# Optimization experiments

Measured on AMD Instinct MI355X. Metric: run time of the kernel, lower is better.

The kernel has to match this reference:

```python
import jax, jax.numpy as jnp
import numpy as np

N_HEADS = 16
D_K = 64
D_V = 64
HIDDEN = 1024
B, S = 2, 2048
LN_EPS = 1e-5


def setup_inputs() -> dict:
    key = jax.random.key(0)
    ks = jax.random.split(key, 6)
    inputs = jax.random.normal(ks[0], (B, S, HIDDEN), dtype=jnp.float32)
    attn_mask = jax.random.randint(ks[1], (B, S, S), 0, 2, dtype=jnp.int32)
    scale = 1.0 / np.sqrt(HIDDEN)
    W_Q = jax.random.normal(ks[2], (HIDDEN, HIDDEN), dtype=jnp.float32) * scale
    W_K = jax.random.normal(ks[3], (HIDDEN, HIDDEN), dtype=jnp.float32) * scale
    W_V = jax.random.normal(ks[4], (HIDDEN, HIDDEN), dtype=jnp.float32) * scale
    W_O = jax.random.normal(ks[5], (HIDDEN, HIDDEN), dtype=jnp.float32) * scale
    return {"inputs": inputs, "attn_mask": attn_mask,
            "W_Q": W_Q, "W_K": W_K, "W_V": W_V, "W_O": W_O}


def reference(inputs, attn_mask, W_Q, W_K, W_V, W_O):
    b, s, _ = inputs.shape
    # nn.Linear(bias=False): x @ W.T ; reshape to [B, H, S, d]
    Q = (inputs @ W_Q.T).reshape(b, s, N_HEADS, D_K).transpose(0, 2, 1, 3)
    K = (inputs @ W_K.T).reshape(b, s, N_HEADS, D_K).transpose(0, 2, 1, 3)
    V = (inputs @ W_V.T).reshape(b, s, N_HEADS, D_V).transpose(0, 2, 1, 3)
    scores = jnp.einsum('bhqd,bhkd->bhqk', Q, K) / np.sqrt(D_K)
    mask = (attn_mask == 0)[:, None, :, :]  # broadcast over heads
    scores = jnp.where(mask, jnp.float32(-1e9), scores)
    attn = jax.nn.softmax(scores, axis=-1)
    context = jnp.einsum('bhqk,bhkd->bhqd', attn, V)
    context = context.transpose(0, 2, 1, 3).reshape(b, s, N_HEADS * D_V)
    output = context @ W_O.T
    x = output + inputs  # residual
    # LayerNorm with default weight=1, bias=0, eps=1e-5
    mu = jnp.mean(x, axis=-1, keepdims=True)
    var = jnp.mean(jnp.square(x - mu), axis=-1, keepdims=True)
    out = (x - mu) * jax.lax.rsqrt(var + LN_EPS)
    return out, attn
```

## Files before the change

kernel.cpp:

```cpp
#include <hip/hip_runtime.h>

typedef unsigned short u16;
typedef unsigned long long u64;
typedef __bf16 bf16x8 __attribute__((ext_vector_type(8)));
typedef float f32x4 __attribute__((ext_vector_type(4)));

static __device__ __forceinline__ u16 f32_to_bf16(float f) {
    unsigned u = __builtin_bit_cast(unsigned, f);
    u += 0x7fffu + ((u >> 16) & 1u);
    return (u16)(u >> 16);
}
static __device__ __forceinline__ float bf16_to_f32(u16 v) {
    return __builtin_bit_cast(float, ((unsigned)v) << 16);
}

__global__ __launch_bounds__(256) void cast_f32_bf16(const float* __restrict__ in,
                                                     u16* __restrict__ out, int n)
{
    int i = (blockIdx.x * 256 + threadIdx.x) * 4;
    if (i >= n) return;
    float4 v = *reinterpret_cast<const float4*>(in + i);
    ushort4 o;
    o.x = f32_to_bf16(v.x); o.y = f32_to_bf16(v.y);
    o.z = f32_to_bf16(v.z); o.w = f32_to_bf16(v.w);
    *reinterpret_cast<ushort4*>(out + i) = o;
}

__global__ __launch_bounds__(256) void cast_w4(
    const float* __restrict__ w0, const float* __restrict__ w1,
    const float* __restrict__ w2, const float* __restrict__ w3,
    u16* __restrict__ o0, u16* __restrict__ o1,
    u16* __restrict__ o2, u16* __restrict__ o3)
{
    const float* src; u16* dst;
    switch (blockIdx.y) {
        case 0: src = w0; dst = o0; break;
        case 1: src = w1; dst = o1; break;
        case 2: src = w2; dst = o2; break;
        default: src = w3; dst = o3; break;
    }
    int i = (blockIdx.x * 256 + threadIdx.x) * 4;
    float4 v = *reinterpret_cast<const float4*>(src + i);
    ushort4 o;
    o.x = f32_to_bf16(v.x); o.y = f32_to_bf16(v.y);
    o.z = f32_to_bf16(v.z); o.w = f32_to_bf16(v.w);
    *reinterpret_cast<ushort4*>(dst + i) = o;
}

__global__ __launch_bounds__(256) void pack_mask(const int* __restrict__ mask,
                                                 u64* __restrict__ out)
{
    int t = blockIdx.x * 256 + threadIdx.x;
    const int4* p = reinterpret_cast<const int4*>(mask + (size_t)t * 64);
    u64 bits = 0;
#pragma unroll
    for (int j = 0; j < 16; ++j) {
        int4 v = p[j];
        bits |= ((u64)(v.x != 0)) << (j * 4 + 0);
        bits |= ((u64)(v.y != 0)) << (j * 4 + 1);
        bits |= ((u64)(v.z != 0)) << (j * 4 + 2);
        bits |= ((u64)(v.w != 0)) << (j * 4 + 3);
    }
    out[t] = bits;
}

__global__ __launch_bounds__(256) void gemm128_qkv(
    const u16* __restrict__ A,
    const u16* __restrict__ BQ, const u16* __restrict__ BK, const u16* __restrict__ BV,
    u16* __restrict__ CQ, u16* __restrict__ CK, u16* __restrict__ CV)
{
    constexpr int N = 1024, K = 1024;
    const u16* B; u16* C;
    switch (blockIdx.z) {
        case 0:  B = BQ; C = CQ; break;
        case 1:  B = BK; C = CK; break;
        default: B = BV; C = CV; break;
    }
    __shared__ __align__(16) u16 As[128][72];
    __shared__ __align__(16) u16 Bs[128][72];
    const int tid  = threadIdx.x;
    const int wave = tid >> 6, lane = tid & 63;
    const int quad = lane >> 4, l16 = lane & 15;
    const int wr = wave >> 1, wc = wave & 1;
    const int m0 = blockIdx.y * 128, n0 = blockIdx.x * 128;

    f32x4 acc[4][4] = {};
    const int r0 = tid >> 3;
    const int c0 = (tid & 7) * 8;
    const u16* Ap = A + (size_t)(m0 + r0) * K + c0;
    const u16* Bp = B + (size_t)(n0 + r0) * K + c0;

    for (int k0 = 0; k0 < K; k0 += 64) {
        __syncthreads();
#pragma unroll
        for (int i = 0; i < 4; ++i) {
            *reinterpret_cast<int4*>(&As[r0 + 32 * i][c0]) =
                *reinterpret_cast<const int4*>(Ap + (size_t)(32 * i) * K + k0);
            *reinterpret_cast<int4*>(&Bs[r0 + 32 * i][c0]) =
                *reinterpret_cast<const int4*>(Bp + (size_t)(32 * i) * K + k0);
        }
        __syncthreads();
#pragma unroll
        for (int ks = 0; ks < 2; ++ks) {
            bf16x8 a[4], bb[4];
#pragma unroll
            for (int mi = 0; mi < 4; ++mi)
                a[mi] = *reinterpret_cast<const bf16x8*>(&As[wr * 64 + mi * 16 + l16][ks * 32 + quad * 8]);
#pragma unroll
            for (int ni = 0; ni < 4; ++ni)
                bb[ni] = *reinterpret_cast<const bf16x8*>(&Bs[wc * 64 + ni * 16 + l16][ks * 32 + quad * 8]);
#pragma unroll
            for (int mi = 0; mi < 4; ++mi)
#pragma unroll
                for (int ni = 0; ni < 4; ++ni)
                    acc[mi][ni] = __builtin_amdgcn_mfma_f32_16x16x32_bf16(a[mi], bb[ni], acc[mi][ni], 0, 0, 0);
        }
    }
#pragma unroll
    for (int mi = 0; mi < 4; ++mi)
#pragma unroll
        for (int ni = 0; ni < 4; ++ni)
#pragma unroll
            for (int r = 0; r < 4; ++r) {
                int row = m0 + wr * 64 + mi * 16 + quad * 4 + r;
                int col = n0 + wc * 64 + ni * 16 + l16;
                C[(size_t)row * N + col] = f32_to_bf16(acc[mi][ni][r]);
            }
}

__global__ __launch_bounds__(256) void gemm128_res(
    const u16* __restrict__ A, const u16* __restrict__ B,
    const float* __restrict__ X, float* __restrict__ C)
{
    constexpr int N = 1024, K = 1024;
    __shared__ __align__(16) u16 As[128][72];
    __shared__ __align__(16) u16 Bs[128][72];
    const int tid  = threadIdx.x;
    const int wave = tid >> 6, lane = tid & 63;
    const int quad = lane >> 4, l16 = lane & 15;
    const int wr = wave >> 1, wc = wave & 1;
    const int m0 = blockIdx.y * 128, n0 = blockIdx.x * 128;

    f32x4 acc[4][4] = {};
    const int r0 = tid >> 3;
    const int c0 = (tid & 7) * 8;
    const u16* Ap = A + (size_t)(m0 + r0) * K + c0;
    const u16* Bp = B + (size_t)(n0 + r0) * K + c0;

    for (int k0 = 0; k0 < K; k0 += 64) {
        __syncthreads();
#pragma unroll
        for (int i = 0; i < 4; ++i) {
            *reinterpret_cast<int4*>(&As[r0 + 32 * i][c0]) =
                *reinterpret_cast<const int4*>(Ap + (size_t)(32 * i) * K + k0);
            *reinterpret_cast<int4*>(&Bs[r0 + 32 * i][c0]) =
                *reinterpret_cast<const int4*>(Bp + (size_t)(32 * i) * K + k0);
        }
        __syncthreads();
#pragma unroll
        for (int ks = 0; ks < 2; ++ks) {
            bf16x8 a[4], bb[4];
#pragma unroll
            for (int mi = 0; mi < 4; ++mi)
                a[mi] = *reinterpret_cast<const bf16x8*>(&As[wr * 64 + mi * 16 + l16][ks * 32 + quad * 8]);
#pragma unroll
            for (int ni = 0; ni < 4; ++ni)
                bb[ni] = *reinterpret_cast<const bf16x8*>(&Bs[wc * 64 + ni * 16 + l16][ks * 32 + quad * 8]);
#pragma unroll
            for (int mi = 0; mi < 4; ++mi)
#pragma unroll
                for (int ni = 0; ni < 4; ++ni)
                    acc[mi][ni] = __builtin_amdgcn_mfma_f32_16x16x32_bf16(a[mi], bb[ni], acc[mi][ni], 0, 0, 0);
        }
    }
#pragma unroll
    for (int mi = 0; mi < 4; ++mi)
#pragma unroll
        for (int ni = 0; ni < 4; ++ni)
#pragma unroll
            for (int r = 0; r < 4; ++r) {
                int row = m0 + wr * 64 + mi * 16 + quad * 4 + r;
                int col = n0 + wc * 64 + ni * 16 + l16;
                C[(size_t)row * N + col] = acc[mi][ni][r] + X[(size_t)row * N + col];
            }
}

__global__ __launch_bounds__(256) void transpose_v(const u16* __restrict__ Vw,
                                                   u16* __restrict__ VT)
{
    constexpr int S = 2048, HID = 1024, NH = 16;
    __shared__ __align__(16) u16 Ts[64][72];
    const int tid = threadIdx.x;
    const int lr = tid >> 2, lc = (tid & 3) * 16;
    const int st = blockIdx.x, h = blockIdx.y, b = blockIdx.z;
    {
        const u16* p = Vw + ((size_t)(b * S + st * 64 + lr)) * HID + h * 64 + lc;
        *reinterpret_cast<int4*>(&Ts[lr][lc])     = *reinterpret_cast<const int4*>(p);
        *reinterpret_cast<int4*>(&Ts[lr][lc + 8]) = *reinterpret_cast<const int4*>(p + 8);
    }
    __syncthreads();
    u16* q = VT + ((size_t)((b * NH + h) * 64 + lr)) * S + st * 64 + lc;
    union { int4 v; u16 s[8]; } o0, o1;
#pragma unroll
    for (int j = 0; j < 8; ++j) o0.s[j] = Ts[lc + j][lr];
#pragma unroll
    for (int j = 0; j < 8; ++j) o1.s[j] = Ts[lc + 8 + j][lr];
    *reinterpret_cast<int4*>(q)     = o0.v;
    *reinterpret_cast<int4*>(q + 8) = o1.v;
}

__global__ __launch_bounds__(256) void attn_kernel(
    const u16* __restrict__ Q, const u16* __restrict__ K,
    const u16* __restrict__ VT, const u64* __restrict__ Mb,
    float* __restrict__ attn_out, u16* __restrict__ ctx_out)
{
    constexpr int S = 2048, HID = 1024, NH = 16;
    __shared__ __align__(16) u16 Qs[64][72];
    __shared__ __align__(16) u16 Ks[64][72];
    __shared__ __align__(16) u16 Vs[64][72];
    __shared__ __align__(16) u16 Ps[64][72];

    const int tid  = threadIdx.x;
    const int wave = tid >> 6, lane = tid & 63;
    const int quad = lane >> 4, l16 = lane & 15;
    const int qt = blockIdx.x, h = blockIdx.y, b = blockIdx.z;
    const size_t qkv_base = (size_t)b * S * HID + h * 64;
    const size_t vt_base  = ((size_t)(b * NH + h)) * 64 * S;

    const int lr = tid >> 2;
    const int lc = (tid & 3) * 16;
    {
        const u16* p = Q + qkv_base + (size_t)(qt * 64 + lr) * HID + lc;
        *reinterpret_cast<int4*>(&Qs[lr][lc])     = *reinterpret_cast<const int4*>(p);
        *reinterpret_cast<int4*>(&Qs[lr][lc + 8]) = *reinterpret_cast<const int4*>(p + 8);
    }

    float m_i[4], l_i[4];
#pragma unroll
    for (int r = 0; r < 4; ++r) { m_i[r] = -1e30f; l_i[r] = 0.f; }

    const int q_row0 = qt * 64 + wave * 16 + quad * 4;
    const size_t mrow = (size_t)b * S + q_row0;

    for (int kt = 0; kt < S / 64; ++kt) {
        u64 mw[4];
#pragma unroll
        for (int r = 0; r < 4; ++r) mw[r] = Mb[(mrow + r) * 32 + kt];
        __syncthreads();
        {
            const u16* p = K + qkv_base + (size_t)(kt * 64 + lr) * HID + lc;
            *reinterpret_cast<int4*>(&Ks[lr][lc])     = *reinterpret_cast<const int4*>(p);
            *reinterpret_cast<int4*>(&Ks[lr][lc + 8]) = *reinterpret_cast<const int4*>(p + 8);
        }
        __syncthreads();
        f32x4 sc[4] = {};
#pragma unroll
        for (int ks = 0; ks < 2; ++ks) {
            bf16x8 a = *reinterpret_cast<const bf16x8*>(&Qs[wave * 16 + l16][ks * 32 + quad * 8]);
#pragma unroll
            for (int cb = 0; cb < 4; ++cb) {
                bf16x8 bb = *reinterpret_cast<const bf16x8*>(&Ks[cb * 16 + l16][ks * 32 + quad * 8]);
                sc[cb] = __builtin_amdgcn_mfma_f32_16x16x32_bf16(a, bb, sc[cb], 0, 0, 0);
            }
        }
        float s_val[4][4];
#pragma unroll
        for (int cb = 0; cb < 4; ++cb) {
            int bi = cb * 16 + l16;
#pragma unroll
            for (int r = 0; r < 4; ++r)
                s_val[cb][r] = ((mw[r] >> bi) & 1ull) ? sc[cb][r] * 0.125f : -1e9f;
        }
#pragma unroll
        for (int r = 0; r < 4; ++r) {
            float mx = fmaxf(fmaxf(s_val[0][r], s_val[1][r]), fmaxf(s_val[2][r], s_val[3][r]));
            mx = fmaxf(mx, __shfl_xor(mx, 1));
            mx = fmaxf(mx, __shfl_xor(mx, 2));
            mx = fmaxf(mx, __shfl_xor(mx, 4));
            mx = fmaxf(mx, __shfl_xor(mx, 8));
            float m_new = fmaxf(m_i[r], mx);
            float sum = 0.f;
#pragma unroll
            for (int cb = 0; cb < 4; ++cb) sum += __expf(s_val[cb][r] - m_new);
            sum += __shfl_xor(sum, 1);
            sum += __shfl_xor(sum, 2);
            sum += __shfl_xor(sum, 4);
            sum += __shfl_xor(sum, 8);
            l_i[r] = l_i[r] * __expf(m_i[r] - m_new) + sum;
            m_i[r] = m_new;
        }
    }
    float rl[4];
#pragma unroll
    for (int r = 0; r < 4; ++r) rl[r] = 1.0f / l_i[r];

    f32x4 ctx[4] = {};
    for (int kt = 0; kt < S / 64; ++kt) {
        u64 mw[4];
#pragma unroll
        for (int r = 0; r < 4; ++r) mw[r] = Mb[(mrow + r) * 32 + kt];
        __syncthreads();
        {
            const u16* p = K + qkv_base + (size_t)(kt * 64 + lr) * HID + lc;
            *reinterpret_cast<int4*>(&Ks[lr][lc])     = *reinterpret_cast<const int4*>(p);
            *reinterpret_cast<int4*>(&Ks[lr][lc + 8]) = *reinterpret_cast<const int4*>(p + 8);
            const u16* pv = VT + vt_base + (size_t)lr * S + kt * 64 + lc;
            *reinterpret_cast<int4*>(&Vs[lr][lc])     = *reinterpret_cast<const int4*>(pv);
            *reinterpret_cast<int4*>(&Vs[lr][lc + 8]) = *reinterpret_cast<const int4*>(pv + 8);
        }
        __syncthreads();
        f32x4 sc[4] = {};
#pragma unroll
        for (int ks = 0; ks < 2; ++ks) {
            bf16x8 a = *reinterpret_cast<const bf16x8*>(&Qs[wave * 16 + l16][ks * 32 + quad * 8]);
#pragma unroll
            for (int cb = 0; cb < 4; ++cb) {
                bf16x8 bb = *reinterpret_cast<const bf16x8*>(&Ks[cb * 16 + l16][ks * 32 + quad * 8]);
                sc[cb] = __builtin_amdgcn_mfma_f32_16x16x32_bf16(a, bb, sc[cb], 0, 0, 0);
            }
        }
#pragma unroll
        for (int cb = 0; cb < 4; ++cb) {
            int bi = cb * 16 + l16;
#pragma unroll
            for (int r = 0; r < 4; ++r) {
                float s = ((mw[r] >> bi) & 1ull) ? sc[cb][r] * 0.125f : -1e9f;
                float pval = __expf(s - m_i[r]) * rl[r];
                Ps[wave * 16 + quad * 4 + r][cb * 16 + l16] = f32_to_bf16(pval);
            }
        }
        __syncthreads();
        {
            size_t arow = (((size_t)(b * NH + h) * S) + qt * 64 + lr) * S + kt * 64 + lc;
#pragma unroll
            for (int g = 0; g < 4; ++g) {
                float4 o;
                o.x = bf16_to_f32(Ps[lr][lc + g * 4 + 0]);
                o.y = bf16_to_f32(Ps[lr][lc + g * 4 + 1]);
                o.z = bf16_to_f32(Ps[lr][lc + g * 4 + 2]);
                o.w = bf16_to_f32(Ps[lr][lc + g * 4 + 3]);
                *reinterpret_cast<float4*>(&attn_out[arow + g * 4]) = o;
            }
        }
#pragma unroll
        for (int ks = 0; ks < 2; ++ks) {
            bf16x8 a = *reinterpret_cast<const bf16x8*>(&Ps[wave * 16 + l16][ks * 32 + quad * 8]);
#pragma unroll
            for (int cb = 0; cb < 4; ++cb) {
                bf16x8 bb = *reinterpret_cast<const bf16x8*>(&Vs[cb * 16 + l16][ks * 32 + quad * 8]);
                ctx[cb] = __builtin_amdgcn_mfma_f32_16x16x32_bf16(a, bb, ctx[cb], 0, 0, 0);
            }
        }
    }
#pragma unroll
    for (int cb = 0; cb < 4; ++cb)
#pragma unroll
        for (int r = 0; r < 4; ++r) {
            int q = q_row0 + r;
            int d = cb * 16 + l16;
            ctx_out[qkv_base + (size_t)q * HID + d] = f32_to_bf16(ctx[cb][r]);
        }
}

__global__ __launch_bounds__(256) void ln_kernel(const float* __restrict__ X,
                                                 float* __restrict__ out)
{
    __shared__ float red[8];
    const int row = blockIdx.x;
    const int tid = threadIdx.x;
    const int wave = tid >> 6, lane = tid & 63;
    const float* xr = X + (size_t)row * 1024;
    float v[4];
    float s = 0.f;
#pragma unroll
    for (int i = 0; i < 4; ++i) { v[i] = xr[tid + 256 * i]; s += v[i]; }
#pragma unroll
    for (int off = 1; off < 64; off <<= 1) s += __shfl_xor(s, off);
    if (lane == 0) red[wave] = s;
    __syncthreads();
    float mean = (red[0] + red[1] + red[2] + red[3]) * (1.0f / 1024.0f);
    float s2 = 0.f;
#pragma unroll
    for (int i = 0; i < 4; ++i) { float d = v[i] - mean; s2 += d * d; }
#pragma unroll
    for (int off = 1; off < 64; off <<= 1) s2 += __shfl_xor(s2, off);
    if (lane == 0) red[4 + wave] = s2;
    __syncthreads();
    float var = (red[4] + red[5] + red[6] + red[7]) * (1.0f / 1024.0f);
    float rstd = rsqrtf(var + 1e-5f);
#pragma unroll
    for (int i = 0; i < 4; ++i)
        out[(size_t)row * 1024 + tid + 256 * i] = (v[i] - mean) * rstd;
}

extern "C" void kernel_launch(void* const* d_in, const int* in_sizes, int n_in,
                              void* d_out, int out_size, void* d_ws, size_t ws_size,
                              hipStream_t stream)
{
    constexpr int B = 2, S = 2048, HID = 1024, NH = 16;
    constexpr int M = B * S;

    const float* X  = (const float*)d_in[0];
    const int* mask = (const int*)d_in[1];
    const float* WQ = (const float*)d_in[2];
    const float* WK = (const float*)d_in[3];
    const float* WV = (const float*)d_in[4];
    const float* WO = (const float*)d_in[5];

    float* out  = (float*)d_out;
    float* attn = out + (size_t)M * HID;

    u64*   Mb  = (u64*)d_ws;
    u16*   Xb  = (u16*)(Mb + (size_t)B * S * 32);
    u16*   WQb = Xb  + (size_t)M * HID;
    u16*   WKb = WQb + (size_t)HID * HID;
    u16*   WVb = WKb + (size_t)HID * HID;
    u16*   WOb = WVb + (size_t)HID * HID;
    u16*   Qw  = WOb + (size_t)HID * HID;
    u16*   Kw  = Qw  + (size_t)M * HID;
    u16*   Vw  = Kw  + (size_t)M * HID;
    u16*   Cw  = Vw  + (size_t)M * HID;
    u16*   VT  = Xb;
    float* XO  = (float*)Qw;

    dim3 blk(256);
    cast_f32_bf16<<<dim3((M * HID) / 1024), blk, 0, stream>>>(X, Xb, M * HID);
    cast_w4<<<dim3((HID * HID) / 1024, 4), blk, 0, stream>>>(WQ, WK, WV, WO,
                                                             WQb, WKb, WVb, WOb);
    pack_mask<<<dim3((B * S * 32) / 256), blk, 0, stream>>>(mask, Mb);

    gemm128_qkv<<<dim3(HID / 128, M / 128, 3), blk, 0, stream>>>(Xb, WQb, WKb, WVb,
                                                                 Qw, Kw, Vw);
    transpose_v<<<dim3(S / 64, NH, B), blk, 0, stream>>>(Vw, VT);

    attn_kernel<<<dim3(S / 64, NH, B), blk, 0, stream>>>(Qw, Kw, VT, Mb, attn, Cw);

    gemm128_res<<<dim3(HID / 128, M / 128), blk, 0, stream>>>(Cw, WOb, X, XO);
    ln_kernel<<<dim3(M), blk, 0, stream>>>(XO, out);
}
```

Before: 889.3 us.

## Prefetch next K/V tiles into registers and swizzle block order across XCDs

The attention kernel now issues the global loads for the next K (and V) tile into registers before computing on the current tile, so memory latency overlaps with the MFMA and softmax work. It also remaps the flat block index so that consecutive hardware block IDs, which are spread round-robin across the chip's chiplets, correspond to nearby (batch, head, q-tile) work. The aim is better L2 locality for the K/V data shared by q-tiles of the same head. The cost is extra live registers for the prefetched tiles, which could lower occupancy.

```diff
diff --git a/kernel.cpp b/kernel.cpp
--- a/kernel.cpp
+++ b/kernel.cpp
@@ -223,7 +223,11 @@
     const int tid  = threadIdx.x;
     const int wave = tid >> 6, lane = tid & 63;
     const int quad = lane >> 4, l16 = lane & 15;
-    const int qt = blockIdx.x, h = blockIdx.y, b = blockIdx.z;
+
+    const int flat = (blockIdx.z * NH + blockIdx.y) * (S / 64) + blockIdx.x;
+    const int s_id = (flat & 7) * 128 + (flat >> 3);
+    const int qt = s_id & 31, h = (s_id >> 5) & 15, b = s_id >> 9;
+
     const size_t qkv_base = (size_t)b * S * HID + h * 64;
     const size_t vt_base  = ((size_t)(b * NH + h)) * 64 * S;
 
@@ -242,16 +246,24 @@
     const int q_row0 = qt * 64 + wave * 16 + quad * 4;
     const size_t mrow = (size_t)b * S + q_row0;
 
+    const u16* Kp = K + qkv_base + (size_t)lr * HID + lc;
+    const u16* Vp = VT + vt_base + (size_t)lr * S + lc;
+
+    int4 kc0 = *reinterpret_cast<const int4*>(Kp);
+    int4 kc1 = *reinterpret_cast<const int4*>(Kp + 8);
     for (int kt = 0; kt < S / 64; ++kt) {
         u64 mw[4];
 #pragma unroll
         for (int r = 0; r < 4; ++r) mw[r] = Mb[(mrow + r) * 32 + kt];
         __syncthreads();
-        {
-            const u16* p = K + qkv_base + (size_t)(kt * 64 + lr) * HID + lc;
-            *reinterpret_cast<int4*>(&Ks[lr][lc])     = *reinterpret_cast<const int4*>(p);
-            *reinterpret_cast<int4*>(&Ks[lr][lc + 8]) = *reinterpret_cast<const int4*>(p + 8);
-        }
+        *reinterpret_cast<int4*>(&Ks[lr][lc])     = kc0;
+        *reinterpret_cast<int4*>(&Ks[lr][lc + 8]) = kc1;
+        int4 kn0, kn1;
+        if (kt < S / 64 - 1) {
+            const u16* p = Kp + (size_t)(kt + 1) * 64 * HID;
+            kn0 = *reinterpret_cast<const int4*>(p);
+            kn1 = *reinterpret_cast<const int4*>(p + 8);
+        } else { kn0 = kc0; kn1 = kc1; }
         __syncthreads();
         f32x4 sc[4] = {};
 #pragma unroll
@@ -289,25 +301,35 @@
             l_i[r] = l_i[r] * __expf(m_i[r] - m_new) + sum;
             m_i[r] = m_new;
         }
+        kc0 = kn0; kc1 = kn1;
     }
     float rl[4];
 #pragma unroll
     for (int r = 0; r < 4; ++r) rl[r] = 1.0f / l_i[r];
 
     f32x4 ctx[4] = {};
+    kc0 = *reinterpret_cast<const int4*>(Kp);
+    kc1 = *reinterpret_cast<const int4*>(Kp + 8);
+    int4 vc0 = *reinterpret_cast<const int4*>(Vp);
+    int4 vc1 = *reinterpret_cast<const int4*>(Vp + 8);
     for (int kt = 0; kt < S / 64; ++kt) {
         u64 mw[4];
 #pragma unroll
         for (int r = 0; r < 4; ++r) mw[r] = Mb[(mrow + r) * 32 + kt];
         __syncthreads();
-        {
-            const u16* p = K + qkv_base + (size_t)(kt * 64 + lr) * HID + lc;
-            *reinterpret_cast<int4*>(&Ks[lr][lc])     = *reinterpret_cast<const int4*>(p);
-            *reinterpret_cast<int4*>(&Ks[lr][lc + 8]) = *reinterpret_cast<const int4*>(p + 8);
-            const u16* pv = VT + vt_base + (size_t)lr * S + kt * 64 + lc;
-            *reinterpret_cast<int4*>(&Vs[lr][lc])     = *reinterpret_cast<const int4*>(pv);
-            *reinterpret_cast<int4*>(&Vs[lr][lc + 8]) = *reinterpret_cast<const int4*>(pv + 8);
-        }
+        *reinterpret_cast<int4*>(&Ks[lr][lc])     = kc0;
+        *reinterpret_cast<int4*>(&Ks[lr][lc + 8]) = kc1;
+        *reinterpret_cast<int4*>(&Vs[lr][lc])     = vc0;
+        *reinterpret_cast<int4*>(&Vs[lr][lc + 8]) = vc1;
+        int4 kn0, kn1, vn0, vn1;
+        if (kt < S / 64 - 1) {
+            const u16* p = Kp + (size_t)(kt + 1) * 64 * HID;
+            kn0 = *reinterpret_cast<const int4*>(p);
+            kn1 = *reinterpret_cast<const int4*>(p + 8);
+            const u16* pv = Vp + (kt + 1) * 64;
+            vn0 = *reinterpret_cast<const int4*>(pv);
+            vn1 = *reinterpret_cast<const int4*>(pv + 8);
+        } else { kn0 = kc0; kn1 = kc1; vn0 = vc0; vn1 = vc1; }
         __syncthreads();
         f32x4 sc[4] = {};
 #pragma unroll
@@ -351,6 +373,7 @@
                 ctx[cb] = __builtin_amdgcn_mfma_f32_16x16x32_bf16(a, bb, ctx[cb], 0, 0, 0);
             }
         }
+        kc0 = kn0; kc1 = kn1; vc0 = vn0; vc1 = vn1;
     }
 #pragma unroll
     for (int cb = 0; cb < 4; ++cb)
```

Result: faster. 854.2 us (-3.9%).
